# Optimization experiments

Measured on AMD Instinct MI355X. Metric: run time of the kernel, lower is better.

## Reference

```python
import jax, jax.numpy as jnp
import numpy as np

T, B, F, H = 256, 128, 1024, 1024  # time (orig dim0), batch (orig dim1), input, hidden


def _xavier(key, shape):
    fan_in, fan_out = shape
    limit = float(np.sqrt(6.0 / (fan_in + fan_out)))
    return jax.random.uniform(key, shape, jnp.float32, -limit, limit)


def setup_inputs() -> dict:
    key = jax.random.key(0)
    k1, k2, k3 = jax.random.split(key, 3)
    return {
        "x": jax.random.normal(k1, (T, B, F), dtype=jnp.float32),
        "h0": jnp.zeros((H,), jnp.float32),
        "c0": jnp.zeros((H,), jnp.float32),
        "weight_ih": _xavier(k2, (F, 4 * H)),
        "weight_hh": _xavier(k3, (H, 4 * H)),
        "bias": jnp.zeros((4 * H,), jnp.float32),
    }


def reference(x, h0, c0, weight_ih, weight_hh, bias):
    # Faithful to the torch code: due to its transpose+index quirk, the
    # recurrence runs over the ORIGINAL dim 0 (time=T) with dim 1 as batch.
    hs = H
    h_init = jnp.broadcast_to(h0, (B, hs))
    c_init = jnp.broadcast_to(c0, (B, hs))

    def step(carry, x_t):  # x_t: (B, F)
        h, c = carry
        gates = x_t @ weight_ih + h @ weight_hh + bias  # (B, 4H)
        i = jax.nn.sigmoid(gates[:, :hs])
        f = jax.nn.sigmoid(gates[:, hs:2 * hs])
        g = jnp.tanh(gates[:, 2 * hs:3 * hs])
        o = jax.nn.sigmoid(gates[:, 3 * hs:])
        c_new = f * c + i * g
        h_new = o * jnp.tanh(c_new)
        return (h_new, c_new), h_new

    (h_t, c_t), hidden_seq = jax.lax.scan(step, (h_init, c_init), x)
    return hidden_seq, h_t, c_t  # hidden_seq: (T, B, H)
```

## Files before the change

kernel.cpp:

```cpp
#include <hip/hip_runtime.h>
#include <hip/hip_bf16.h>


typedef __attribute__((ext_vector_type(8))) short short8;
typedef __attribute__((ext_vector_type(4))) float floatx4;

#define HID_OFF 33554432L
#define CT_OFF  33685504L
#define WTAIL_F 29360128L

__device__ __forceinline__ unsigned short f2bf(float f) {
    __hip_bfloat16 hb = __float2bfloat16(f);
    return *reinterpret_cast<unsigned short*>(&hb);
}

__device__ __forceinline__ uint4 pack8(const float* p) {
    float4 f0 = *reinterpret_cast<const float4*>(p);
    float4 f1 = *reinterpret_cast<const float4*>(p + 4);
    union { uint4 v; unsigned short u[8]; } t;
    t.u[0] = f2bf(f0.x); t.u[1] = f2bf(f0.y); t.u[2] = f2bf(f0.z); t.u[3] = f2bf(f0.w);
    t.u[4] = f2bf(f1.x); t.u[5] = f2bf(f1.y); t.u[6] = f2bf(f1.z); t.u[7] = f2bf(f1.w);
    return t.v;
}

__global__ void pack_w_kernel(const float* __restrict__ wih,
                              const float* __restrict__ whh,
                              unsigned short* __restrict__ pB) {
    int g    = blockIdx.x * 256 + threadIdx.x;
    int lane = g & 63;
    int frag = g >> 6;
    int kblk = frag & 63;
    int nblk = frag >> 6;
    int n = nblk * 16 + (lane & 15);
    int k = kblk * 32 + ((lane >> 4) << 3);
    const float* src = (k < 1024) ? (wih + (size_t)k * 4096 + n)
                                  : (whh + (size_t)(k - 1024) * 4096 + n);
    __attribute__((aligned(16))) unsigned short tmp[8];
#pragma unroll
    for (int jj = 0; jj < 8; ++jj) tmp[jj] = f2bf(src[(size_t)jj * 4096]);
    *reinterpret_cast<uint4*>(pB + (size_t)frag * 512 + lane * 8) =
        *reinterpret_cast<const uint4*>(tmp);
}

__global__ void pack_x_kernel(const float* __restrict__ x,
                              unsigned short* __restrict__ pX) {
    int g    = blockIdx.x * 256 + threadIdx.x;
    int lane = g & 63;
    int frag = g >> 6;
    int kblk = frag & 31;
    int mblk = (frag >> 5) & 7;
    int t    = frag >> 8;
    int m = mblk * 16 + (lane & 15);
    int k = kblk * 32 + ((lane >> 4) << 3);
    *reinterpret_cast<uint4*>(pX + (size_t)frag * 512 + lane * 8) =
        pack8(x + (size_t)(t * 128 + m) * 1024 + k);
}

__global__ __launch_bounds__(256, 1) void lstm_main(
    const float* __restrict__ x, const float* __restrict__ h0,
    const float* __restrict__ c0, const float* __restrict__ bias,
    const unsigned short* __restrict__ pB,
    unsigned short* pH, int use_ph,
    const unsigned short* __restrict__ pX, int use_px,
    float* out, int* cnt) {

    __shared__ __align__(16) unsigned short Abuf[2][32][512];
    __shared__ float g_lds[4][32][17];
    __shared__ float c_lds[32][16];
    __shared__ __align__(16) unsigned short hbf_lds[32][16];

    const int tid  = threadIdx.x;
    const int lane = tid & 63;
    const int w    = tid >> 6;
    const int wg   = blockIdx.x;
    const int r    = (wg >> 3) & 3;
    const int j    = (wg & 7) * 8 + (wg >> 5);
    const int col  = lane & 15;
    const int quad = lane >> 4;
    const int nblk = w * 64 + j;

    int* subp = cnt + (r * 8 + (j >> 3)) * 64;

    const float breg = bias[w * 1024 + j * 16 + col];

    {
        float cv = c0[j * 16 + (tid & 15)];
        int row = tid >> 4;
        c_lds[row][tid & 15]      = cv;
        c_lds[row + 16][tid & 15] = cv;
    }

    const unsigned short* pBw = pB + (size_t)nblk * 64 * 512 + lane * 8;
    short8 bw[64];
#pragma unroll
    for (int kb = 0; kb < 64; ++kb)
        bw[kb] = *reinterpret_cast<const short8*>(pBw + (size_t)kb * 512);

    auto stage_x_full = [&](int tt) {
#pragma unroll
        for (int i = 0; i < 16; ++i) {
            int s = tid + 256 * i;
            int ln = s & 63, kbg = (s >> 6) & 31, mb = s >> 11;
            if (use_px) {
                const unsigned short* src =
                    pX + (((size_t)(tt * 8 + 2 * r + mb) * 32 + kbg) * 512) + ln * 8;
                *reinterpret_cast<uint4*>(&Abuf[mb][kbg][ln * 8]) =
                    *reinterpret_cast<const uint4*>(src);
            } else {
                int m = 32 * r + mb * 16 + (ln & 15);
                int k = kbg * 32 + ((ln >> 4) << 3);
                *reinterpret_cast<uint4*>(&Abuf[mb][kbg][ln * 8]) =
                    pack8(x + (size_t)(tt * 128 + m) * 1024 + k);
            }
        }
    };

    auto stage_h_full = [&](int tt) {
        if (tt == 0) {
#pragma unroll
            for (int i = 0; i < 16; ++i) {
                int s = tid + 256 * i;
                int ln = s & 63, kbg = (s >> 6) & 31, mb = s >> 11;
                int k = kbg * 32 + ((ln >> 4) << 3);
                union { uint4 v; unsigned short u[8]; } tv;
#pragma unroll
                for (int jj = 0; jj < 8; ++jj) tv.u[jj] = f2bf(h0[k + jj]);
                *reinterpret_cast<uint4*>(&Abuf[mb][kbg][ln * 8]) = tv.v;
            }
        } else if (use_ph) {
            const unsigned long long* hb = reinterpret_cast<const unsigned long long*>(
                pH + (size_t)(tt & 1) * 131072);
            unsigned long long v[32];
#pragma unroll
            for (int i = 0; i < 16; ++i) {
                int s = tid + 256 * i;
                int ln = s & 63, kbg = (s >> 6) & 31, mb = s >> 11;
                size_t u = (((size_t)(2 * r + mb) * 32 + kbg) * 512 + ln * 8) >> 2;
                v[2 * i]     = __hip_atomic_load(hb + u, __ATOMIC_RELAXED,
                                                 __HIP_MEMORY_SCOPE_AGENT);
                v[2 * i + 1] = __hip_atomic_load(hb + u + 1, __ATOMIC_RELAXED,
                                                 __HIP_MEMORY_SCOPE_AGENT);
            }
#pragma unroll
            for (int i = 0; i < 16; ++i) {
                int s = tid + 256 * i;
                int ln = s & 63, kbg = (s >> 6) & 31, mb = s >> 11;
                unsigned long long* dp =
                    reinterpret_cast<unsigned long long*>(&Abuf[mb][kbg][ln * 8]);
                dp[0] = v[2 * i];
                dp[1] = v[2 * i + 1];
            }
        } else {
#pragma unroll
            for (int i = 0; i < 16; ++i) {
                int s = tid + 256 * i;
                int ln = s & 63, kbg = (s >> 6) & 31, mb = s >> 11;
                int m = 32 * r + mb * 16 + (ln & 15);
                int k = kbg * 32 + ((ln >> 4) << 3);
                *reinterpret_cast<uint4*>(&Abuf[mb][kbg][ln * 8]) =
                    pack8(out + (size_t)(tt - 1) * 131072 + (size_t)m * 1024 + k);
            }
        }
    };

    auto gemm_x = [&](floatx4& A0, floatx4& A1) {
#pragma unroll
        for (int kb = 0; kb < 32; ++kb) {
            short8 a0 = *reinterpret_cast<const short8*>(&Abuf[0][kb][lane * 8]);
            short8 a1 = *reinterpret_cast<const short8*>(&Abuf[1][kb][lane * 8]);
            A0 = __builtin_amdgcn_mfma_f32_16x16x32_bf16(a0, bw[kb], A0, 0, 0, 0);
            A1 = __builtin_amdgcn_mfma_f32_16x16x32_bf16(a1, bw[kb], A1, 0, 0, 0);
        }
    };
    auto gemm_h = [&](floatx4& A0, floatx4& A1) {
#pragma unroll
        for (int kb = 0; kb < 32; ++kb) {
            short8 a0 = *reinterpret_cast<const short8*>(&Abuf[0][kb][lane * 8]);
            short8 a1 = *reinterpret_cast<const short8*>(&Abuf[1][kb][lane * 8]);
            A0 = __builtin_amdgcn_mfma_f32_16x16x32_bf16(a0, bw[32 + kb], A0, 0, 0, 0);
            A1 = __builtin_amdgcn_mfma_f32_16x16x32_bf16(a1, bw[32 + kb], A1, 0, 0, 0);
        }
    };

    floatx4 xa0 = {0.f, 0.f, 0.f, 0.f}, xa1 = {0.f, 0.f, 0.f, 0.f};

    __syncthreads();
    stage_x_full(0);
    __syncthreads();
    gemm_x(xa0, xa1);

    for (int t = 0; t < 256; ++t) {
        floatx4 acc0 = xa0, acc1 = xa1;

        if (t > 0 && tid < 8) {
            int* sp = cnt + (r * 8 + tid) * 64;
            const int target = 8 * t;
            while (true) {
                int vv = __hip_atomic_load(sp, __ATOMIC_RELAXED,
                                           __HIP_MEMORY_SCOPE_AGENT);
                if (__ballot(vv >= target) == 0xFFull) break;
                __builtin_amdgcn_s_sleep(1);
            }
            if (!use_ph)
                __builtin_amdgcn_fence(__ATOMIC_ACQUIRE, "agent");
        }
        __syncthreads();

        stage_h_full(t);
        __syncthreads();
        gemm_h(acc0, acc1);

#pragma unroll
        for (int rr = 0; rr < 4; ++rr) {
            float p0 = acc0[rr] + breg;
            float p1 = acc1[rr] + breg;
            float v0, v1;
            if (w == 2) { v0 = tanhf(p0); v1 = tanhf(p1); }
            else        { v0 = 1.f / (1.f + __expf(-p0)); v1 = 1.f / (1.f + __expf(-p1)); }
            g_lds[w][quad * 4 + rr][col]      = v0;
            g_lds[w][16 + quad * 4 + rr][col] = v1;
        }
        __syncthreads();

        const int row0 = tid >> 4, cc = tid & 15;
        float hv0, hv1, cn0, cn1;
        {
            float iv = g_lds[0][row0][cc];
            float fv = g_lds[1][row0][cc];
            float gv = g_lds[2][row0][cc];
            float ov = g_lds[3][row0][cc];
            cn0 = fv * c_lds[row0][cc] + iv * gv;
            hv0 = ov * tanhf(cn0);
            c_lds[row0][cc]   = cn0;
            hbf_lds[row0][cc] = f2bf(hv0);
            int row1 = row0 + 16;
            iv = g_lds[0][row1][cc];
            fv = g_lds[1][row1][cc];
            gv = g_lds[2][row1][cc];
            ov = g_lds[3][row1][cc];
            cn1 = fv * c_lds[row1][cc] + iv * gv;
            hv1 = ov * tanhf(cn1);
            c_lds[row1][cc]   = cn1;
            hbf_lds[row1][cc] = f2bf(hv1);
        }
        __syncthreads();

        auto store_out = [&]() {
            const long hidbase = (long)t * 131072;
            const long m0 = 32 * r + row0, m1 = m0 + 16;
            out[hidbase + m0 * 1024 + j * 16 + cc] = hv0;
            out[hidbase + m1 * 1024 + j * 16 + cc] = hv1;
            if (t == 255) {
                out[HID_OFF + m0 * 1024 + j * 16 + cc] = hv0;
                out[HID_OFF + m1 * 1024 + j * 16 + cc] = hv1;
                out[CT_OFF  + m0 * 1024 + j * 16 + cc] = cn0;
                out[CT_OFF  + m1 * 1024 + j * 16 + cc] = cn1;
            }
        };

        if (!use_ph) store_out();

        if (t < 255) {
            if (use_ph && tid < 64) {
                int ml = tid >> 1, cg = tid & 1;
                int m = 32 * r + ml, kcol = j * 16 + cg * 8;
                int frag  = (2 * r + (ml >> 4)) * 32 + (kcol >> 5);
                int lanep = (m & 15) + 16 * ((kcol & 31) >> 3);
                unsigned short* dst = pH + (size_t)((t & 1) ^ 1) * 131072 +
                                      (size_t)frag * 512 + lanep * 8;
                const unsigned long long* sv =
                    reinterpret_cast<const unsigned long long*>(&hbf_lds[ml][cg * 8]);
                unsigned long long* d64 = reinterpret_cast<unsigned long long*>(dst);
                __hip_atomic_store(d64, sv[0], __ATOMIC_RELAXED,
                                   __HIP_MEMORY_SCOPE_AGENT);
                __hip_atomic_store(d64 + 1, sv[1], __ATOMIC_RELAXED,
                                   __HIP_MEMORY_SCOPE_AGENT);
            }
            if (tid == 0) {
                if (use_ph) {
                    asm volatile("s_waitcnt vmcnt(0)" ::: "memory");
                    __hip_atomic_fetch_add(subp, 1, __ATOMIC_RELAXED,
                                           __HIP_MEMORY_SCOPE_AGENT);
                } else {
                    __hip_atomic_fetch_add(subp, 1, __ATOMIC_RELEASE,
                                           __HIP_MEMORY_SCOPE_AGENT);
                }
            }
        }

        if (use_ph) store_out();

        if (t < 255) {
            xa0 = (floatx4){0.f, 0.f, 0.f, 0.f};
            xa1 = (floatx4){0.f, 0.f, 0.f, 0.f};
            stage_x_full(t + 1);
            __syncthreads();
            gemm_x(xa0, xa1);
        }
    }
}

extern "C" void kernel_launch(void* const* d_in, const int* in_sizes, int n_in,
                              void* d_out, int out_size, void* d_ws, size_t ws_size,
                              hipStream_t stream) {
    (void)in_sizes; (void)n_in; (void)out_size;
    const float* x    = (const float*)d_in[0];
    const float* h0   = (const float*)d_in[1];
    const float* c0   = (const float*)d_in[2];
    const float* wih  = (const float*)d_in[3];
    const float* whh  = (const float*)d_in[4];
    const float* bias = (const float*)d_in[5];
    float* out = (float*)d_out;

    char* ws = (char*)d_ws;
    int* counters = (int*)ws;
    const size_t SZB = 2048ull * 4096 * 2;
    const size_t SZH = 2ull * 256 * 512 * 2;
    const size_t SZX = 65536ull * 512 * 2;

    size_t off = 16384;
    unsigned short* pB;
    if (ws_size >= off + SZB) {
        pB = (unsigned short*)(ws + off); off += SZB;
    } else {
        pB = (unsigned short*)(out + WTAIL_F);
    }
    int use_ph = (ws_size >= off + SZH) ? 1 : 0;
    unsigned short* pH = use_ph ? (unsigned short*)(ws + off) : (unsigned short*)0;
    if (use_ph) off += SZH;
    int use_px = (ws_size >= off + SZX) ? 1 : 0;
    unsigned short* pX = use_px ? (unsigned short*)(ws + off) : (unsigned short*)0;

    hipMemsetAsync(ws, 0, 16384, stream);
    pack_w_kernel<<<4096, 256, 0, stream>>>(wih, whh, pB);
    if (use_px) pack_x_kernel<<<16384, 256, 0, stream>>>(x, pX);

    lstm_main<<<dim3(256), dim3(256), 0, stream>>>(
        x, h0, c0, bias, pB, pH, use_ph, pX, use_px, out, counters);
}
```

Before: 3.231 ms.

## Overlap recurrent h load latency with input-projection MFMA via split LDS buffers

Splits the shared A buffer into separate X and H buffers. After the counter wait, each step issues non-temporal global loads of the packed h tile into registers, then runs the x-projection GEMM while those loads are in flight, and only then writes h into LDS and runs the h GEMM. Staging of the next x tile moves to the end of the step with a lighter barrier. The aim is to hide global load latency on the serial critical path, at the cost of doubled LDS use and more live registers alongside the 64 resident weight fragments. The x GEMM now sits after the wait instead of being precomputed before it, so it is on the critical path unless the overlap covers it.

New measurement: 3.203 ms. No clear change (-0.9%).

```diff
diff --git a/kernel.cpp b/kernel.cpp
--- a/kernel.cpp
+++ b/kernel.cpp
@@ -64,7 +64,8 @@
     const unsigned short* __restrict__ pX, int use_px,
     float* out, int* cnt) {
 
-    __shared__ __align__(16) unsigned short Abuf[2][32][512];
+    __shared__ __align__(16) unsigned short AbufX[2][32][512];
+    __shared__ __align__(16) unsigned short AbufH[2][32][512];
     __shared__ float g_lds[4][32][17];
     __shared__ float c_lds[32][16];
     __shared__ __align__(16) unsigned short hbf_lds[32][16];
@@ -104,70 +105,47 @@
             if (use_px) {
                 const unsigned short* src =
                     pX + (((size_t)(tt * 8 + 2 * r + mb) * 32 + kbg) * 512) + ln * 8;
-                *reinterpret_cast<uint4*>(&Abuf[mb][kbg][ln * 8]) =
+                *reinterpret_cast<uint4*>(&AbufX[mb][kbg][ln * 8]) =
                     *reinterpret_cast<const uint4*>(src);
             } else {
                 int m = 32 * r + mb * 16 + (ln & 15);
                 int k = kbg * 32 + ((ln >> 4) << 3);
-                *reinterpret_cast<uint4*>(&Abuf[mb][kbg][ln * 8]) =
+                *reinterpret_cast<uint4*>(&AbufX[mb][kbg][ln * 8]) =
                     pack8(x + (size_t)(tt * 128 + m) * 1024 + k);
             }
         }
     };
 
-    auto stage_h_full = [&](int tt) {
-        if (tt == 0) {
-#pragma unroll
-            for (int i = 0; i < 16; ++i) {
-                int s = tid + 256 * i;
-                int ln = s & 63, kbg = (s >> 6) & 31, mb = s >> 11;
-                int k = kbg * 32 + ((ln >> 4) << 3);
-                union { uint4 v; unsigned short u[8]; } tv;
-#pragma unroll
-                for (int jj = 0; jj < 8; ++jj) tv.u[jj] = f2bf(h0[k + jj]);
-                *reinterpret_cast<uint4*>(&Abuf[mb][kbg][ln * 8]) = tv.v;
-            }
-        } else if (use_ph) {
-            const unsigned long long* hb = reinterpret_cast<const unsigned long long*>(
-                pH + (size_t)(tt & 1) * 131072);
-            unsigned long long v[32];
-#pragma unroll
-            for (int i = 0; i < 16; ++i) {
-                int s = tid + 256 * i;
-                int ln = s & 63, kbg = (s >> 6) & 31, mb = s >> 11;
-                size_t u = (((size_t)(2 * r + mb) * 32 + kbg) * 512 + ln * 8) >> 2;
-                v[2 * i]     = __hip_atomic_load(hb + u, __ATOMIC_RELAXED,
-                                                 __HIP_MEMORY_SCOPE_AGENT);
-                v[2 * i + 1] = __hip_atomic_load(hb + u + 1, __ATOMIC_RELAXED,
-                                                 __HIP_MEMORY_SCOPE_AGENT);
-            }
-#pragma unroll
-            for (int i = 0; i < 16; ++i) {
-                int s = tid + 256 * i;
-                int ln = s & 63, kbg = (s >> 6) & 31, mb = s >> 11;
-                unsigned long long* dp =
-                    reinterpret_cast<unsigned long long*>(&Abuf[mb][kbg][ln * 8]);
-                dp[0] = v[2 * i];
-                dp[1] = v[2 * i + 1];
-            }
-        } else {
-#pragma unroll
-            for (int i = 0; i < 16; ++i) {
-                int s = tid + 256 * i;
-                int ln = s & 63, kbg = (s >> 6) & 31, mb = s >> 11;
-                int m = 32 * r + mb * 16 + (ln & 15);
-                int k = kbg * 32 + ((ln >> 4) << 3);
-                *reinterpret_cast<uint4*>(&Abuf[mb][kbg][ln * 8]) =
-                    pack8(out + (size_t)(tt - 1) * 131072 + (size_t)m * 1024 + k);
-            }
+    auto stage_h0 = [&]() {
+#pragma unroll
+        for (int i = 0; i < 16; ++i) {
+            int s = tid + 256 * i;
+            int ln = s & 63, kbg = (s >> 6) & 31, mb = s >> 11;
+            int k = kbg * 32 + ((ln >> 4) << 3);
+            union { uint4 v; unsigned short u[8]; } tv;
+#pragma unroll
+            for (int jj = 0; jj < 8; ++jj) tv.u[jj] = f2bf(h0[k + jj]);
+            *reinterpret_cast<uint4*>(&AbufH[mb][kbg][ln * 8]) = tv.v;
+        }
+    };
+
+    auto stage_h_out = [&](int tt) {
+#pragma unroll
+        for (int i = 0; i < 16; ++i) {
+            int s = tid + 256 * i;
+            int ln = s & 63, kbg = (s >> 6) & 31, mb = s >> 11;
+            int m = 32 * r + mb * 16 + (ln & 15);
+            int k = kbg * 32 + ((ln >> 4) << 3);
+            *reinterpret_cast<uint4*>(&AbufH[mb][kbg][ln * 8]) =
+                pack8(out + (size_t)(tt - 1) * 131072 + (size_t)m * 1024 + k);
         }
     };
 
     auto gemm_x = [&](floatx4& A0, floatx4& A1) {
 #pragma unroll
         for (int kb = 0; kb < 32; ++kb) {
-            short8 a0 = *reinterpret_cast<const short8*>(&Abuf[0][kb][lane * 8]);
-            short8 a1 = *reinterpret_cast<const short8*>(&Abuf[1][kb][lane * 8]);
+            short8 a0 = *reinterpret_cast<const short8*>(&AbufX[0][kb][lane * 8]);
+            short8 a1 = *reinterpret_cast<const short8*>(&AbufX[1][kb][lane * 8]);
             A0 = __builtin_amdgcn_mfma_f32_16x16x32_bf16(a0, bw[kb], A0, 0, 0, 0);
             A1 = __builtin_amdgcn_mfma_f32_16x16x32_bf16(a1, bw[kb], A1, 0, 0, 0);
         }
@@ -175,23 +153,19 @@
     auto gemm_h = [&](floatx4& A0, floatx4& A1) {
 #pragma unroll
         for (int kb = 0; kb < 32; ++kb) {
-            short8 a0 = *reinterpret_cast<const short8*>(&Abuf[0][kb][lane * 8]);
-            short8 a1 = *reinterpret_cast<const short8*>(&Abuf[1][kb][lane * 8]);
+            short8 a0 = *reinterpret_cast<const short8*>(&AbufH[0][kb][lane * 8]);
+            short8 a1 = *reinterpret_cast<const short8*>(&AbufH[1][kb][lane * 8]);
             A0 = __builtin_amdgcn_mfma_f32_16x16x32_bf16(a0, bw[32 + kb], A0, 0, 0, 0);
             A1 = __builtin_amdgcn_mfma_f32_16x16x32_bf16(a1, bw[32 + kb], A1, 0, 0, 0);
         }
     };
 
-    floatx4 xa0 = {0.f, 0.f, 0.f, 0.f}, xa1 = {0.f, 0.f, 0.f, 0.f};
-
     __syncthreads();
     stage_x_full(0);
-    __syncthreads();
-    gemm_x(xa0, xa1);
+    asm volatile("s_waitcnt lgkmcnt(0)" ::: "memory");
+    __builtin_amdgcn_s_barrier();
 
     for (int t = 0; t < 256; ++t) {
-        floatx4 acc0 = xa0, acc1 = xa1;
-
         if (t > 0 && tid < 8) {
             int* sp = cnt + (r * 8 + tid) * 64;
             const int target = 8 * t;
@@ -204,10 +178,36 @@
             if (!use_ph)
                 __builtin_amdgcn_fence(__ATOMIC_ACQUIRE, "agent");
         }
+        __builtin_amdgcn_s_barrier();
+
+        uint4 hreg[16];
+        if (t == 0) {
+            stage_h0();
+        } else if (use_ph) {
+            const char* bb = (const char*)pH + (size_t)(t & 1) * 262144 +
+                             (size_t)r * 65536 + (tid >> 6) * 1024 + (tid & 63) * 16;
+#pragma unroll
+            for (int i = 0; i < 16; ++i)
+                asm volatile("global_load_dwordx4 %0, %1, off sc0 sc1"
+                             : "=v"(hreg[i]) : "v"(bb + (size_t)i * 4096) : "memory");
+        } else {
+            stage_h_out(t);
+        }
+
+        floatx4 acc0 = {0.f, 0.f, 0.f, 0.f}, acc1 = {0.f, 0.f, 0.f, 0.f};
+        gemm_x(acc0, acc1);
+
+        if (t > 0 && use_ph) {
+            __builtin_amdgcn_sched_barrier(0);
+            asm volatile("s_waitcnt vmcnt(0)" ::: "memory");
+            __builtin_amdgcn_sched_barrier(0);
+            unsigned short* ld = &AbufH[0][0][0] + (tid >> 6) * 512 + (tid & 63) * 8;
+#pragma unroll
+            for (int i = 0; i < 16; ++i)
+                *reinterpret_cast<uint4*>(ld + i * 2048) = hreg[i];
+        }
         __syncthreads();
 
-        stage_h_full(t);
-        __syncthreads();
         gemm_h(acc0, acc1);
 
 #pragma unroll
@@ -290,13 +290,9 @@
 
         if (use_ph) store_out();
 
-        if (t < 255) {
-            xa0 = (floatx4){0.f, 0.f, 0.f, 0.f};
-            xa1 = (floatx4){0.f, 0.f, 0.f, 0.f};
-            stage_x_full(t + 1);
-            __syncthreads();
-            gemm_x(xa0, xa1);
-        }
+        if (t < 255) stage_x_full(t + 1);
+        asm volatile("s_waitcnt lgkmcnt(0)" ::: "memory");
+        __builtin_amdgcn_s_barrier();
     }
 }
 
```
